# Performance work log

Measured on AMD Instinct MI355X. Metric: run time of the kernel, lower is better.

Reference implementation:

```python
import jax, jax.numpy as jnp
import numpy as np

SEF = 64   # skipped edge features (MLPGraphNetwork default sef)
SNF = 64   # skipped node features (MLPGraphNetwork default snf)
NR_STEPS = 3


def mlp2(x, W0, b0, W1, b1):
    # MyMLP with multI=1.0, relu hidden, linear last, no layernorm
    return jax.nn.relu(x @ W0 + b0) @ W1 + b1


def setup_inputs() -> dict:
    N, E = 50000, 800000
    nrNodeF, nrEdgeF, nrEmbed, nrTypes = 32, 3, 16, 2
    key = jax.random.key(0)
    ks = jax.random.split(key, 20)

    def w(k, fi, fo):
        # torch.normal(0,1) * (2.0 / fan_in)  (relu init in MyMLP)
        return jax.random.normal(k, (fi, fo), jnp.float32) * (2.0 / fi)

    z = lambda n: jnp.zeros((n,), jnp.float32)
    return {
        "edge_index": jax.random.randint(ks[0], (2, E), 0, N),
        "nodeFeatures": jax.random.uniform(ks[1], (N, nrNodeF), jnp.float32),
        "edgeFeatures": jax.random.normal(ks[2], (E, nrEdgeF), jnp.float32),
        "emb": jax.random.normal(ks[3], (nrTypes, nrEmbed), jnp.float32),
        "enc_n_W0": w(ks[4], nrNodeF - 1 + nrEmbed, 128), "enc_n_b0": z(128),
        "enc_n_W1": w(ks[5], 128, 128), "enc_n_b1": z(128),
        "enc_e_W0": w(ks[6], nrEdgeF, 128), "enc_e_b0": z(128),
        "enc_e_W1": w(ks[7], 128, 128), "enc_e_b1": z(128),
        "core_e_W0": w(ks[8], 192, 128), "core_e_b0": z(128),
        "core_e_W1": w(ks[9], 128, 64), "core_e_b1": z(64),
        "core_n_W0": w(ks[10], 128, 128), "core_n_b0": z(128),
        "core_n_W1": w(ks[11], 128, 64), "core_n_b1": z(64),
        "dec_W0": w(ks[12], 128, 128), "dec_b0": z(128),
        "dec_W1": w(ks[13], 128, 3), "dec_b1": z(3),
    }


def reference(edge_index, nodeFeatures, edgeFeatures, emb,
              enc_n_W0, enc_n_b0, enc_n_W1, enc_n_b1,
              enc_e_W0, enc_e_b0, enc_e_W1, enc_e_b1,
              core_e_W0, core_e_b0, core_e_W1, core_e_b1,
              core_n_W0, core_n_b0, core_n_W1, core_n_b1,
              dec_W0, dec_b0, dec_W1, dec_b1):
    N = nodeFeatures.shape[0]
    src, dst = edge_index[0], edge_index[1]  # j (source), i (target)

    # encode: embed particle type from last node feature column
    ptype = (nodeFeatures[:, -1] + 0.5).astype(jnp.int32)
    node = jnp.concatenate([nodeFeatures[:, :-1], emb[ptype]], axis=-1)
    node = mlp2(node, enc_n_W0, enc_n_b0, enc_n_W1, enc_n_b1)          # [N,128]
    edge = mlp2(edgeFeatures, enc_e_W0, enc_e_b0, enc_e_W1, enc_e_b1)  # [E,128]

    ones = jnp.ones((edge_index.shape[1],), node.dtype)
    counts = jnp.maximum(jax.ops.segment_sum(ones, dst, num_segments=N), 1.0)

    # process: shared MLPGraphNetwork applied NR_STEPS times
    for _ in range(NR_STEPS):
        einp = jnp.concatenate([edge[:, SEF:], node[dst][:, SNF:], node[src][:, SNF:]], axis=-1)  # [E,192]
        eout = mlp2(einp, core_e_W0, core_e_b0, core_e_W1, core_e_b1)  # [E,64]
        edge = jnp.concatenate([edge[:, :SEF], edge[:, SEF:] + eout], axis=-1)  # residual tail, [E,128]
        agg = jax.ops.segment_sum(edge, dst, num_segments=N) / counts[:, None]  # mean aggr, [N,128]
        ninp = jnp.concatenate([agg[:, SEF:], node[:, SNF:]], axis=-1)  # [N,128]
        nout = mlp2(ninp, core_n_W0, core_n_b0, core_n_W1, core_n_b1)  # [N,64]
        node = jnp.concatenate([node[:, :SNF], node[:, SNF:] + nout], axis=-1)  # [N,128]

    # decode
    return mlp2(node, dec_W0, dec_b0, dec_W1, dec_b1)  # [N,3]
```

## Files before the change

kernel.cpp:

```cpp
#include <hip/hip_runtime.h>
#include <cstdint>
#include <cstddef>


__global__ void k_zero(int* __restrict__ p, int n) {
    int i = blockIdx.x * 256 + threadIdx.x;
    if (i < n) p[i] = 0;
}


__global__ void k_hist(const int* __restrict__ dst, int* __restrict__ counts, int E) {
    int e = blockIdx.x * 256 + threadIdx.x;
    if (e < E) atomicAdd(&counts[dst[e]], 1);
}

__global__ __launch_bounds__(1024) void k_scan(
    const int* __restrict__ counts, int* __restrict__ row_off,
    int* __restrict__ cursor, float* __restrict__ inv_cnt, int N) {
    __shared__ int wsum[16];
    int t = threadIdx.x;
    int wave = t >> 6, lane = t & 63;
    int carry = 0;
    for (int base = 0; base < N; base += 1024) {
        int i = base + t;
        int v = (i < N) ? counts[i] : 0;
        int s = v;
        #pragma unroll
        for (int off = 1; off < 64; off <<= 1) {
            int u = __shfl_up(s, off, 64);
            if (lane >= off) s += u;
        }
        if (lane == 63) wsum[wave] = s;
        __syncthreads();
        int wpre = 0, full = 0;
        #pragma unroll
        for (int wv = 0; wv < 16; wv++) {
            int x = wsum[wv];
            full += x;
            if (wv < wave) wpre += x;
        }
        if (i < N) {
            int excl = carry + wpre + s - v;
            row_off[i] = excl;
            cursor[i]  = excl;
            inv_cnt[i] = 1.0f / (float)((v > 0) ? v : 1);
        }
        carry += full;
        __syncthreads();
    }
    if (t == 0) row_off[N] = carry;
}

__global__ void k_fill(const int* __restrict__ dst, int* __restrict__ cursor,
                       int* __restrict__ edge_list, int E) {
    int e = blockIdx.x * 256 + threadIdx.x;
    if (e < E) {
        int pos = atomicAdd(&cursor[dst[e]], 1);
        edge_list[pos] = e;
    }
}

__global__ void k_perm_idx(const int* __restrict__ elist,
                           const int* __restrict__ src, const int* __restrict__ dst,
                           int* __restrict__ src_p, int* __restrict__ dst_p, int E) {
    int i = blockIdx.x * 256 + threadIdx.x;
    if (i < E) {
        int e = elist[i];
        src_p[i] = src[e];
        dst_p[i] = dst[e];
    }
}


__global__ void k_embW(const float* __restrict__ emb, const float* __restrict__ W0,
                       const float* __restrict__ b0, float* __restrict__ embW) {
    int c = threadIdx.x;
    #pragma unroll
    for (int p = 0; p < 2; p++) {
        float acc = b0[c];
        #pragma unroll
        for (int k = 0; k < 16; k++)
            acc = fmaf(emb[p * 16 + k], W0[(31 + k) * 128 + c], acc);
        embW[p * 128 + c] = acc;
    }
}


__device__ __forceinline__ void g1_accum32(
    const float4* __restrict__ a4, int kk4,
    const float* __restrict__ W, int cbase, float* __restrict__ h) {
    #pragma clang loop unroll(disable)
    for (int kk = 0; kk < kk4; kk++) {
        float4 a = a4[kk];
        const float* wr = W + (size_t)kk * 4 * 128 + cbase;
        const float4* w0 = reinterpret_cast<const float4*>(wr);
        const float4* w1 = reinterpret_cast<const float4*>(wr + 128);
        const float4* w2 = reinterpret_cast<const float4*>(wr + 256);
        const float4* w3 = reinterpret_cast<const float4*>(wr + 384);
        #pragma unroll
        for (int cg = 0; cg < 8; cg++) {
            float4 p = w0[cg], q = w1[cg], r = w2[cg], s = w3[cg];
            h[cg*4+0] = fmaf(a.w, s.x, fmaf(a.z, r.x, fmaf(a.y, q.x, fmaf(a.x, p.x, h[cg*4+0]))));
            h[cg*4+1] = fmaf(a.w, s.y, fmaf(a.z, r.y, fmaf(a.y, q.y, fmaf(a.x, p.y, h[cg*4+1]))));
            h[cg*4+2] = fmaf(a.w, s.z, fmaf(a.z, r.z, fmaf(a.y, q.z, fmaf(a.x, p.z, h[cg*4+2]))));
            h[cg*4+3] = fmaf(a.w, s.w, fmaf(a.z, r.w, fmaf(a.y, q.w, fmaf(a.x, p.w, h[cg*4+3]))));
        }
    }
}

__device__ __forceinline__ void g1_tail3(
    float x, float y, float z, const float* __restrict__ W, int cbase,
    float* __restrict__ h) {
    const float4* w0 = reinterpret_cast<const float4*>(W + cbase);
    const float4* w1 = reinterpret_cast<const float4*>(W + 128 + cbase);
    const float4* w2 = reinterpret_cast<const float4*>(W + 256 + cbase);
    #pragma unroll
    for (int cg = 0; cg < 8; cg++) {
        float4 p = w0[cg], q = w1[cg], r = w2[cg];
        h[cg*4+0] = fmaf(z, r.x, fmaf(y, q.x, fmaf(x, p.x, h[cg*4+0])));
        h[cg*4+1] = fmaf(z, r.y, fmaf(y, q.y, fmaf(x, p.y, h[cg*4+1])));
        h[cg*4+2] = fmaf(z, r.z, fmaf(y, q.z, fmaf(x, p.z, h[cg*4+2])));
        h[cg*4+3] = fmaf(z, r.w, fmaf(y, q.w, fmaf(x, p.w, h[cg*4+3])));
    }
}

__device__ __forceinline__ void g2_accum64(
    float* __restrict__ sb, const float* __restrict__ hc,
    const float* __restrict__ W1, int kbase, int rs, float* __restrict__ o) {
    int t = threadIdx.x;
    #pragma unroll
    for (int k = 0; k < 32; k++) sb[k * 256 + t] = hc[k];
    __syncthreads();
    #pragma clang loop unroll(disable)
    for (int k = 0; k < 32; k++) {
        float hk = sb[k * 256 + t];
        const float4* w = reinterpret_cast<const float4*>(W1 + (size_t)(kbase + k) * rs);
        #pragma unroll
        for (int cg = 0; cg < 16; cg++) {
            float4 wv = w[cg];
            o[cg*4+0] = fmaf(hk, wv.x, o[cg*4+0]);
            o[cg*4+1] = fmaf(hk, wv.y, o[cg*4+1]);
            o[cg*4+2] = fmaf(hk, wv.z, o[cg*4+2]);
            o[cg*4+3] = fmaf(hk, wv.w, o[cg*4+3]);
        }
    }
    __syncthreads();
}


__global__ __launch_bounds__(256, 2) void k_enc_node_tail(
    const float* __restrict__ nodeF, const float* __restrict__ embW,
    const float* __restrict__ W0, const float* __restrict__ W1,
    const float* __restrict__ b1, float* __restrict__ nodeT, int N) {
    __shared__ float sb[32 * 256];
    int n = blockIdx.x * 256 + threadIdx.x;
    bool valid = n < N;
    int nc = valid ? n : N - 1;
    const float4* nf4 = reinterpret_cast<const float4*>(nodeF + (size_t)nc * 32);
    float4 v7 = nf4[7];
    int p = (int)(v7.w + 0.5f);
    const float4* ew = reinterpret_cast<const float4*>(embW + p * 128);

    float o[64];
    const float4* bv = reinterpret_cast<const float4*>(b1 + 64);
    #pragma unroll
    for (int i = 0; i < 16; i++) {
        float4 b = bv[i];
        o[4*i+0] = b.x; o[4*i+1] = b.y; o[4*i+2] = b.z; o[4*i+3] = b.w;
    }
    #pragma unroll
    for (int ch = 0; ch < 4; ch++) {
        int cbase = ch * 32;
        float h[32];
        #pragma unroll
        for (int i = 0; i < 8; i++) {
            float4 u = ew[ch*8 + i];
            h[4*i+0] = u.x; h[4*i+1] = u.y; h[4*i+2] = u.z; h[4*i+3] = u.w;
        }
        g1_accum32(nf4, 7, W0, cbase, h);
        g1_tail3(v7.x, v7.y, v7.z, W0 + 28*128, cbase, h);
        #pragma unroll
        for (int i = 0; i < 32; i++) h[i] = fmaxf(h[i], 0.0f);
        g2_accum64(sb, h, W1 + 64, cbase, 128, o);
    }
    if (valid) {
        float4* out4 = reinterpret_cast<float4*>(nodeT + (size_t)n * 64);
        #pragma unroll
        for (int i = 0; i < 16; i++)
            out4[i] = make_float4(o[4*i], o[4*i+1], o[4*i+2], o[4*i+3]);
    }
}


__global__ __launch_bounds__(256, 3) void k_enc_edge_T(
    const float* __restrict__ edgeF, const int* __restrict__ perm, int usePerm,
    const float* __restrict__ W0, const float* __restrict__ b0,
    const float* __restrict__ W1, const float* __restrict__ b1,
    float* __restrict__ edgeT, int E) {
    __shared__ float H[128 * 65];
    __shared__ float Wbuf[32 * 68];
    __shared__ float Xs[64 * 4];

    int t = threadIdx.x;
    int base = blockIdx.x * 64;

    if (t < 192) {
        int i = t / 3, j = t - i * 3;
        int e = base + i; int ec = (e < E) ? e : E - 1;
        int e2 = usePerm ? perm[ec] : ec;
        Xs[i * 4 + j] = edgeF[(size_t)e2 * 3 + j];
    }
    __syncthreads();

    int eg = t & 15, cg = t >> 4;
    float c1[4][8];
    {
        float4 b0a = *reinterpret_cast<const float4*>(b0 + cg * 8);
        float4 b0b = *reinterpret_cast<const float4*>(b0 + cg * 8 + 4);
        float bb[8] = {b0a.x,b0a.y,b0a.z,b0a.w,b0b.x,b0b.y,b0b.z,b0b.w};
        #pragma unroll
        for (int ie = 0; ie < 4; ie++)
            #pragma unroll
            for (int jc = 0; jc < 8; jc++) c1[ie][jc] = bb[jc];
    }
    #pragma unroll
    for (int k = 0; k < 3; k++) {
        float4 wa = *reinterpret_cast<const float4*>(W0 + k * 128 + cg * 8);
        float4 wb = *reinterpret_cast<const float4*>(W0 + k * 128 + cg * 8 + 4);
        float ww[8] = {wa.x,wa.y,wa.z,wa.w,wb.x,wb.y,wb.z,wb.w};
        #pragma unroll
        for (int ie = 0; ie < 4; ie++) {
            float a = Xs[(eg + 16 * ie) * 4 + k];
            #pragma unroll
            for (int jc = 0; jc < 8; jc++)
                c1[ie][jc] = fmaf(a, ww[jc], c1[ie][jc]);
        }
    }

    int wr_r = t >> 3, wr_cb = t & 7;
    float4 wreg2[2];
    {
        const float4* wr = reinterpret_cast<const float4*>(
            W1 + (size_t)(wr_r) * 128 + 64 + wr_cb * 8);
        wreg2[0] = wr[0]; wreg2[1] = wr[1];
    }

    #pragma unroll
    for (int ie = 0; ie < 4; ie++)
        #pragma unroll
        for (int jc = 0; jc < 8; jc++)
            H[(cg * 8 + jc) * 65 + eg + 16 * ie] = fmaxf(c1[ie][jc], 0.0f);

    int eg2 = t & 15, cg2 = t >> 4;
    float c2[4][4];
    {
        float4 bv = *reinterpret_cast<const float4*>(b1 + 64 + cg2 * 4);
        #pragma unroll
        for (int ie = 0; ie < 4; ie++) {
            c2[ie][0]=bv.x; c2[ie][1]=bv.y; c2[ie][2]=bv.z; c2[ie][3]=bv.w;
        }
    }
    #pragma clang loop unroll(disable)
    for (int phase = 0; phase < 4; phase++) {
        __syncthreads();
        {
            float* wd = Wbuf + wr_r * 68 + wr_cb * 8;
            wd[0]=wreg2[0].x; wd[1]=wreg2[0].y; wd[2]=wreg2[0].z; wd[3]=wreg2[0].w;
            wd[4]=wreg2[1].x; wd[5]=wreg2[1].y; wd[6]=wreg2[1].z; wd[7]=wreg2[1].w;
        }
        __syncthreads();
        if (phase < 3) {
            const float4* wr = reinterpret_cast<const float4*>(
                W1 + (size_t)((phase + 1) * 32 + wr_r) * 128 + 64 + wr_cb * 8);
            wreg2[0] = wr[0]; wreg2[1] = wr[1];
        }
        #pragma clang loop unroll_count(4)
        for (int k = 0; k < 32; k++) {
            int c = phase * 32 + k;
            float a0 = H[c*65 + eg2*4 + 0];
            float a1 = H[c*65 + eg2*4 + 1];
            float a2 = H[c*65 + eg2*4 + 2];
            float a3 = H[c*65 + eg2*4 + 3];
            float4 b4 = *reinterpret_cast<const float4*>(Wbuf + k * 68 + cg2 * 4);
            float bb[4] = {b4.x, b4.y, b4.z, b4.w};
            #pragma unroll
            for (int jc = 0; jc < 4; jc++) {
                c2[0][jc] = fmaf(a0, bb[jc], c2[0][jc]);
                c2[1][jc] = fmaf(a1, bb[jc], c2[1][jc]);
                c2[2][jc] = fmaf(a2, bb[jc], c2[2][jc]);
                c2[3][jc] = fmaf(a3, bb[jc], c2[3][jc]);
            }
        }
    }
    #pragma unroll
    for (int ie = 0; ie < 4; ie++) {
        int e = base + eg2 * 4 + ie;
        if (e < E) {
            *reinterpret_cast<float4*>(edgeT + (size_t)e * 64 + cg2 * 4) =
                make_float4(c2[ie][0], c2[ie][1], c2[ie][2], c2[ie][3]);
        }
    }
}


__global__ __launch_bounds__(256, 4) void k_node_pre_d(
    const float* __restrict__ nodeT, const float* __restrict__ W0,
    const float* __restrict__ b0, float* __restrict__ Pd, int N) {
    int n = blockIdx.x * 256 + threadIdx.x;
    bool valid = n < N;
    int nc = valid ? n : N - 1;
    const float4* a4 = reinterpret_cast<const float4*>(nodeT + (size_t)nc * 64);

    #pragma unroll
    for (int ch = 0; ch < 4; ch++) {
        int cbase = ch * 32;
        float h[32];
        const float4* b0v = reinterpret_cast<const float4*>(b0 + cbase);
        #pragma unroll
        for (int i = 0; i < 8; i++) {
            float4 b = b0v[i];
            h[4*i+0] = b.x; h[4*i+1] = b.y; h[4*i+2] = b.z; h[4*i+3] = b.w;
        }
        g1_accum32(a4, 16, W0 + 64*128, cbase, h);
        if (valid) {
            float4* o4 = reinterpret_cast<float4*>(Pd + (size_t)n * 128 + cbase);
            #pragma unroll
            for (int i = 0; i < 8; i++)
                o4[i] = make_float4(h[4*i], h[4*i+1], h[4*i+2], h[4*i+3]);
        }
    }
}


__global__ __launch_bounds__(256, 3) void k_edge_core_T(
    float* __restrict__ edgeT, const float* __restrict__ Pd,
    const float* __restrict__ nodeT,
    const int* __restrict__ srcI, const int* __restrict__ dstI,
    const float* __restrict__ W0, const float* __restrict__ W1,
    const float* __restrict__ b1, int E) {
    __shared__ float Abuf[2 * 64 * 65];
    __shared__ float Wbuf[32 * 132];

    int t = threadIdx.x;
    int base = blockIdx.x * 64;

    {
        int i = t >> 2, q = t & 3;
        int e = base + i; int ec = (e < E) ? e : E - 1;
        const float4* er = reinterpret_cast<const float4*>(edgeT + (size_t)ec * 64 + q * 16);
        int s = srcI[ec];
        const float4* sr = reinterpret_cast<const float4*>(nodeT + (size_t)s * 64 + q * 16);
        float* ae = Abuf + i * 65 + q * 16;
        float* as = Abuf + 64 * 65 + i * 65 + q * 16;
        #pragma unroll
        for (int j4 = 0; j4 < 4; j4++) {
            float4 v = er[j4];
            ae[j4*4+0]=v.x; ae[j4*4+1]=v.y; ae[j4*4+2]=v.z; ae[j4*4+3]=v.w;
            float4 w = sr[j4];
            as[j4*4+0]=w.x; as[j4*4+1]=w.y; as[j4*4+2]=w.z; as[j4*4+3]=w.w;
        }
    }

    int eg = t & 15, cg = t >> 4;
    float c1[4][8];
    #pragma unroll
    for (int ie = 0; ie < 4; ie++) {
        int e = base + eg + 16 * ie; int ec = (e < E) ? e : E - 1;
        int d = dstI[ec];
        const float4* pr = reinterpret_cast<const float4*>(Pd + (size_t)d * 128 + cg * 8);
        float4 p0 = pr[0], p1 = pr[1];
        c1[ie][0]=p0.x; c1[ie][1]=p0.y; c1[ie][2]=p0.z; c1[ie][3]=p0.w;
        c1[ie][4]=p1.x; c1[ie][5]=p1.y; c1[ie][6]=p1.z; c1[ie][7]=p1.w;
    }

    int wr_r = t >> 3, wr_cb = t & 7;
    float4 wreg[4];
    {
        const float4* wr = reinterpret_cast<const float4*>(
            W0 + (size_t)(0 + wr_r) * 128 + wr_cb * 16);
        wreg[0]=wr[0]; wreg[1]=wr[1]; wreg[2]=wr[2]; wreg[3]=wr[3];
    }
    #pragma clang loop unroll(disable)
    for (int phase = 0; phase < 4; phase++) {
        const float* Asrc = Abuf + ((phase < 2) ? 0 : 64 * 65);
        int koff = (phase & 1) * 32;
        __syncthreads();
        {
            float* wd = Wbuf + wr_r * 132 + wr_cb * 16;
            #pragma unroll
            for (int j4 = 0; j4 < 4; j4++) {
                wd[j4*4+0]=wreg[j4].x; wd[j4*4+1]=wreg[j4].y;
                wd[j4*4+2]=wreg[j4].z; wd[j4*4+3]=wreg[j4].w;
            }
        }
        __syncthreads();
        if (phase < 3) {
            int wrow_n = (phase + 1 < 2) ? (phase + 1) * 32 : 128 + (phase - 1) * 32;
            const float4* wr = reinterpret_cast<const float4*>(
                W0 + (size_t)(wrow_n + wr_r) * 128 + wr_cb * 16);
            wreg[0]=wr[0]; wreg[1]=wr[1]; wreg[2]=wr[2]; wreg[3]=wr[3];
        }
        #pragma clang loop unroll_count(4)
        for (int k = 0; k < 32; k++) {
            float a0 = Asrc[(eg + 16*0)*65 + koff + k];
            float a1 = Asrc[(eg + 16*1)*65 + koff + k];
            float a2 = Asrc[(eg + 16*2)*65 + koff + k];
            float a3 = Asrc[(eg + 16*3)*65 + koff + k];
            const float* wrp = Wbuf + k * 132 + cg * 8;
            float4 bq0 = *reinterpret_cast<const float4*>(wrp);
            float4 bq1 = *reinterpret_cast<const float4*>(wrp + 4);
            float bb[8] = {bq0.x,bq0.y,bq0.z,bq0.w,bq1.x,bq1.y,bq1.z,bq1.w};
            #pragma unroll
            for (int jc = 0; jc < 8; jc++) {
                c1[0][jc] = fmaf(a0, bb[jc], c1[0][jc]);
                c1[1][jc] = fmaf(a1, bb[jc], c1[1][jc]);
                c1[2][jc] = fmaf(a2, bb[jc], c1[2][jc]);
                c1[3][jc] = fmaf(a3, bb[jc], c1[3][jc]);
            }
        }
    }

    float4 wreg2[2];
    {
        const float4* wr = reinterpret_cast<const float4*>(
            W1 + (size_t)(wr_r) * 64 + wr_cb * 8);
        wreg2[0] = wr[0]; wreg2[1] = wr[1];
    }

    __syncthreads();
    float* H = Abuf;
    #pragma unroll
    for (int ie = 0; ie < 4; ie++)
        #pragma unroll
        for (int jc = 0; jc < 8; jc++)
            H[(cg*8 + jc) * 65 + eg + 16*ie] = fmaxf(c1[ie][jc], 0.0f);

    int eg2 = t & 15, cg2 = t >> 4;
    float c2[4][4];
    {
        float4 bv = *reinterpret_cast<const float4*>(b1 + cg2 * 4);
        #pragma unroll
        for (int ie = 0; ie < 4; ie++) {
            c2[ie][0]=bv.x; c2[ie][1]=bv.y; c2[ie][2]=bv.z; c2[ie][3]=bv.w;
        }
    }
    #pragma clang loop unroll(disable)
    for (int phase = 0; phase < 4; phase++) {
        __syncthreads();
        {
            float* wd = Wbuf + wr_r * 68 + wr_cb * 8;
            wd[0]=wreg2[0].x; wd[1]=wreg2[0].y; wd[2]=wreg2[0].z; wd[3]=wreg2[0].w;
            wd[4]=wreg2[1].x; wd[5]=wreg2[1].y; wd[6]=wreg2[1].z; wd[7]=wreg2[1].w;
        }
        __syncthreads();
        if (phase < 3) {
            const float4* wr = reinterpret_cast<const float4*>(
                W1 + (size_t)((phase + 1) * 32 + wr_r) * 64 + wr_cb * 8);
            wreg2[0] = wr[0]; wreg2[1] = wr[1];
        }
        #pragma clang loop unroll_count(4)
        for (int k = 0; k < 32; k++) {
            int c = phase * 32 + k;
            float a0 = H[c*65 + eg2*4 + 0];
            float a1 = H[c*65 + eg2*4 + 1];
            float a2 = H[c*65 + eg2*4 + 2];
            float a3 = H[c*65 + eg2*4 + 3];
            float4 b4 = *reinterpret_cast<const float4*>(Wbuf + k * 68 + cg2 * 4);
            float bb[4] = {b4.x, b4.y, b4.z, b4.w};
            #pragma unroll
            for (int jc = 0; jc < 4; jc++) {
                c2[0][jc] = fmaf(a0, bb[jc], c2[0][jc]);
                c2[1][jc] = fmaf(a1, bb[jc], c2[1][jc]);
                c2[2][jc] = fmaf(a2, bb[jc], c2[2][jc]);
                c2[3][jc] = fmaf(a3, bb[jc], c2[3][jc]);
            }
        }
    }

    #pragma unroll
    for (int ie = 0; ie < 4; ie++) {
        int e = base + eg2 * 4 + ie;
        if (e < E) {
            float4* er = reinterpret_cast<float4*>(edgeT + (size_t)e * 64 + cg2 * 4);
            float4 old = *er;
            old.x += c2[ie][0]; old.y += c2[ie][1];
            old.z += c2[ie][2]; old.w += c2[ie][3];
            *er = old;
        }
    }
}


__global__ __launch_bounds__(256, 3) void k_node_core_T(
    const float* __restrict__ aggT, float* __restrict__ nodeT,
    const float* __restrict__ W0, const float* __restrict__ b0,
    const float* __restrict__ W1, const float* __restrict__ b1, int N) {
    __shared__ float Abuf[64 * 132];
    __shared__ float Wbuf[32 * 132];

    int t = threadIdx.x;
    int base = blockIdx.x * 64;

    {
        int i = t >> 2, q = t & 3;
        int n = base + i; int nc = (n < N) ? n : N - 1;
        const float4* gr = reinterpret_cast<const float4*>(aggT + (size_t)nc * 64 + q * 16);
        const float4* tr = reinterpret_cast<const float4*>(nodeT + (size_t)nc * 64 + q * 16);
        float* ag = Abuf + i * 132 + q * 16;
        float* at = Abuf + i * 132 + 64 + q * 16;
        #pragma unroll
        for (int j4 = 0; j4 < 4; j4++) {
            float4 v = gr[j4];
            ag[j4*4+0]=v.x; ag[j4*4+1]=v.y; ag[j4*4+2]=v.z; ag[j4*4+3]=v.w;
            float4 w = tr[j4];
            at[j4*4+0]=w.x; at[j4*4+1]=w.y; at[j4*4+2]=w.z; at[j4*4+3]=w.w;
        }
    }

    int ng = t & 15, cg = t >> 4;
    float c1[4][8];
    {
        float4 b0a = *reinterpret_cast<const float4*>(b0 + cg * 8);
        float4 b0b = *reinterpret_cast<const float4*>(b0 + cg * 8 + 4);
        float bb[8] = {b0a.x,b0a.y,b0a.z,b0a.w,b0b.x,b0b.y,b0b.z,b0b.w};
        #pragma unroll
        for (int in = 0; in < 4; in++)
            #pragma unroll
            for (int jc = 0; jc < 8; jc++) c1[in][jc] = bb[jc];
    }

    int wr_r = t >> 3, wr_cb = t & 7;
    float4 wreg[4];
    {
        const float4* wr = reinterpret_cast<const float4*>(
            W0 + (size_t)(wr_r) * 128 + wr_cb * 16);
        wreg[0]=wr[0]; wreg[1]=wr[1]; wreg[2]=wr[2]; wreg[3]=wr[3];
    }
    #pragma clang loop unroll(disable)
    for (int phase = 0; phase < 4; phase++) {
        int koff = phase * 32;
        __syncthreads();
        {
            float* wd = Wbuf + wr_r * 132 + wr_cb * 16;
            #pragma unroll
            for (int j4 = 0; j4 < 4; j4++) {
                wd[j4*4+0]=wreg[j4].x; wd[j4*4+1]=wreg[j4].y;
                wd[j4*4+2]=wreg[j4].z; wd[j4*4+3]=wreg[j4].w;
            }
        }
        __syncthreads();
        if (phase < 3) {
            const float4* wr = reinterpret_cast<const float4*>(
                W0 + (size_t)((phase + 1) * 32 + wr_r) * 128 + wr_cb * 16);
            wreg[0]=wr[0]; wreg[1]=wr[1]; wreg[2]=wr[2]; wreg[3]=wr[3];
        }
        #pragma clang loop unroll_count(4)
        for (int k = 0; k < 32; k++) {
            float a0 = Abuf[(ng + 16*0)*132 + koff + k];
            float a1 = Abuf[(ng + 16*1)*132 + koff + k];
            float a2 = Abuf[(ng + 16*2)*132 + koff + k];
            float a3 = Abuf[(ng + 16*3)*132 + koff + k];
            const float* wrp = Wbuf + k * 132 + cg * 8;
            float4 bq0 = *reinterpret_cast<const float4*>(wrp);
            float4 bq1 = *reinterpret_cast<const float4*>(wrp + 4);
            float bb[8] = {bq0.x,bq0.y,bq0.z,bq0.w,bq1.x,bq1.y,bq1.z,bq1.w};
            #pragma unroll
            for (int jc = 0; jc < 8; jc++) {
                c1[0][jc] = fmaf(a0, bb[jc], c1[0][jc]);
                c1[1][jc] = fmaf(a1, bb[jc], c1[1][jc]);
                c1[2][jc] = fmaf(a2, bb[jc], c1[2][jc]);
                c1[3][jc] = fmaf(a3, bb[jc], c1[3][jc]);
            }
        }
    }

    float4 wreg2[2];
    {
        const float4* wr = reinterpret_cast<const float4*>(
            W1 + (size_t)(wr_r) * 64 + wr_cb * 8);
        wreg2[0] = wr[0]; wreg2[1] = wr[1];
    }

    __syncthreads();
    float* H = Abuf;
    #pragma unroll
    for (int in = 0; in < 4; in++)
        #pragma unroll
        for (int jc = 0; jc < 8; jc++)
            H[(cg*8 + jc) * 65 + ng + 16*in] = fmaxf(c1[in][jc], 0.0f);

    int ng2 = t & 15, cg2 = t >> 4;
    float c2[4][4];
    {
        float4 bv = *reinterpret_cast<const float4*>(b1 + cg2 * 4);
        #pragma unroll
        for (int in = 0; in < 4; in++) {
            c2[in][0]=bv.x; c2[in][1]=bv.y; c2[in][2]=bv.z; c2[in][3]=bv.w;
        }
    }
    #pragma clang loop unroll(disable)
    for (int phase = 0; phase < 4; phase++) {
        __syncthreads();
        {
            float* wd = Wbuf + wr_r * 68 + wr_cb * 8;
            wd[0]=wreg2[0].x; wd[1]=wreg2[0].y; wd[2]=wreg2[0].z; wd[3]=wreg2[0].w;
            wd[4]=wreg2[1].x; wd[5]=wreg2[1].y; wd[6]=wreg2[1].z; wd[7]=wreg2[1].w;
        }
        __syncthreads();
        if (phase < 3) {
            const float4* wr = reinterpret_cast<const float4*>(
                W1 + (size_t)((phase + 1) * 32 + wr_r) * 64 + wr_cb * 8);
            wreg2[0] = wr[0]; wreg2[1] = wr[1];
        }
        #pragma clang loop unroll_count(4)
        for (int k = 0; k < 32; k++) {
            int c = phase * 32 + k;
            float a0 = H[c*65 + ng2*4 + 0];
            float a1 = H[c*65 + ng2*4 + 1];
            float a2 = H[c*65 + ng2*4 + 2];
            float a3 = H[c*65 + ng2*4 + 3];
            float4 b4 = *reinterpret_cast<const float4*>(Wbuf + k * 68 + cg2 * 4);
            float bb[4] = {b4.x, b4.y, b4.z, b4.w};
            #pragma unroll
            for (int jc = 0; jc < 4; jc++) {
                c2[0][jc] = fmaf(a0, bb[jc], c2[0][jc]);
                c2[1][jc] = fmaf(a1, bb[jc], c2[1][jc]);
                c2[2][jc] = fmaf(a2, bb[jc], c2[2][jc]);
                c2[3][jc] = fmaf(a3, bb[jc], c2[3][jc]);
            }
        }
    }

    #pragma unroll
    for (int in = 0; in < 4; in++) {
        int n = base + ng2 * 4 + in;
        if (n < N) {
            float4* nr = reinterpret_cast<float4*>(nodeT + (size_t)n * 64 + cg2 * 4);
            float4 old = *nr;
            old.x += c2[in][0]; old.y += c2[in][1];
            old.z += c2[in][2]; old.w += c2[in][3];
            *nr = old;
        }
    }
}


__global__ __launch_bounds__(256, 2) void k_edge_core_B(
    float* __restrict__ edgeT, const float* __restrict__ nodeT,
    const int* __restrict__ src, const int* __restrict__ dst,
    const float* __restrict__ W0, const float* __restrict__ b0,
    const float* __restrict__ W1, const float* __restrict__ b1, int E) {
    __shared__ float sb[32 * 256];
    int e = blockIdx.x * 256 + threadIdx.x;
    bool valid = e < E;
    int ec = valid ? e : E - 1;
    int d = dst[ec], s = src[ec];
    const float4* a4 = reinterpret_cast<const float4*>(edgeT + (size_t)ec * 64);
    const float4* d4 = reinterpret_cast<const float4*>(nodeT + (size_t)d * 64);
    const float4* s4 = reinterpret_cast<const float4*>(nodeT + (size_t)s * 64);

    float o[64];
    const float4* bv = reinterpret_cast<const float4*>(b1);
    #pragma unroll
    for (int i = 0; i < 16; i++) {
        float4 b = bv[i];
        o[4*i+0] = b.x; o[4*i+1] = b.y; o[4*i+2] = b.z; o[4*i+3] = b.w;
    }
    #pragma unroll
    for (int ch = 0; ch < 4; ch++) {
        int cbase = ch * 32;
        float h[32];
        const float4* b0v = reinterpret_cast<const float4*>(b0 + cbase);
        #pragma unroll
        for (int i = 0; i < 8; i++) {
            float4 b = b0v[i];
            h[4*i+0] = b.x; h[4*i+1] = b.y; h[4*i+2] = b.z; h[4*i+3] = b.w;
        }
        g1_accum32(a4, 16, W0, cbase, h);
        g1_accum32(d4, 16, W0 + 64*128, cbase, h);
        g1_accum32(s4, 16, W0 + 128*128, cbase, h);
        #pragma unroll
        for (int i = 0; i < 32; i++) h[i] = fmaxf(h[i], 0.0f);
        g2_accum64(sb, h, W1, cbase, 64, o);
    }
    if (valid) {
        float4* eo4 = reinterpret_cast<float4*>(edgeT + (size_t)e * 64);
        #pragma unroll
        for (int i = 0; i < 16; i++) {
            float4 t = a4[i];
            t.x += o[4*i+0]; t.y += o[4*i+1];
            t.z += o[4*i+2]; t.w += o[4*i+3];
            eo4[i] = t;
        }
    }
}


__global__ __launch_bounds__(256) void k_agg_csr(
    const float* __restrict__ edgeT, const int* __restrict__ row_off,
    const float* __restrict__ inv_cnt, float* __restrict__ aggT, int N) {
    int n = blockIdx.x * 4 + (threadIdx.x >> 6);
    int lane = threadIdx.x & 63;
    if (n >= N) return;
    int beg = row_off[n], end = row_off[n + 1];
    double s = 0.0;
    for (int idx = beg; idx < end; idx++)
        s += (double)edgeT[(size_t)idx * 64 + lane];
    aggT[(size_t)n * 64 + lane] = (float)(s * (double)inv_cnt[n]);
}

__global__ __launch_bounds__(256) void k_agg_gather(
    const float* __restrict__ edgeT, const int* __restrict__ row_off,
    const int* __restrict__ edge_list, const float* __restrict__ inv_cnt,
    float* __restrict__ aggT, int N) {
    int n = blockIdx.x * 4 + (threadIdx.x >> 6);
    int lane = threadIdx.x & 63;
    if (n >= N) return;
    int beg = row_off[n], end = row_off[n + 1];
    double s = 0.0;
    for (int idx = beg; idx < end; idx++) {
        int e = edge_list[idx];
        s += (double)edgeT[(size_t)e * 64 + lane];
    }
    aggT[(size_t)n * 64 + lane] = (float)(s * (double)inv_cnt[n]);
}


__global__ __launch_bounds__(256, 2) void k_decode(
    const float* __restrict__ nodeF, const float* __restrict__ embW,
    const float* __restrict__ encW0, const float* __restrict__ encW1,
    const float* __restrict__ encb1, const float* __restrict__ nodeT,
    const float* __restrict__ W0, const float* __restrict__ b0,
    const float* __restrict__ W1, const float* __restrict__ b1,
    float* __restrict__ out, int N) {
    __shared__ float sb[64 * 256];
    int t = threadIdx.x;
    int n = blockIdx.x * 256 + t;
    bool valid = n < N;
    int nc = valid ? n : N - 1;
    const float4* nf4 = reinterpret_cast<const float4*>(nodeF + (size_t)nc * 32);
    const float4* t4  = reinterpret_cast<const float4*>(nodeT + (size_t)nc * 64);
    float4 v7 = nf4[7];
    int p = (int)(v7.w + 0.5f);
    const float4* ew = reinterpret_cast<const float4*>(embW + p * 128);

    float head[64];
    const float4* ebv = reinterpret_cast<const float4*>(encb1);
    #pragma unroll
    for (int i = 0; i < 16; i++) {
        float4 b = ebv[i];
        head[4*i+0] = b.x; head[4*i+1] = b.y; head[4*i+2] = b.z; head[4*i+3] = b.w;
    }
    #pragma unroll
    for (int ch = 0; ch < 4; ch++) {
        int cbase = ch * 32;
        float h[32];
        #pragma unroll
        for (int i = 0; i < 8; i++) {
            float4 u = ew[ch*8 + i];
            h[4*i+0] = u.x; h[4*i+1] = u.y; h[4*i+2] = u.z; h[4*i+3] = u.w;
        }
        g1_accum32(nf4, 7, encW0, cbase, h);
        g1_tail3(v7.x, v7.y, v7.z, encW0 + 28*128, cbase, h);
        #pragma unroll
        for (int i = 0; i < 32; i++) h[i] = fmaxf(h[i], 0.0f);
        g2_accum64(sb, h, encW1, cbase, 128, head);
    }

    #pragma unroll
    for (int k = 0; k < 64; k++) sb[k * 256 + t] = head[k];
    __syncthreads();

    float h2[128];
    #pragma unroll
    for (int ch = 0; ch < 4; ch++) {
        int cbase = ch * 32;
        float* hc = &h2[ch * 32];
        const float4* b0v = reinterpret_cast<const float4*>(b0 + cbase);
        #pragma unroll
        for (int i = 0; i < 8; i++) {
            float4 b = b0v[i];
            hc[4*i+0] = b.x; hc[4*i+1] = b.y; hc[4*i+2] = b.z; hc[4*i+3] = b.w;
        }
        #pragma clang loop unroll(disable)
        for (int k = 0; k < 64; k++) {
            float hk = sb[k * 256 + t];
            const float4* w = reinterpret_cast<const float4*>(W0 + (size_t)k * 128 + cbase);
            #pragma unroll
            for (int cg = 0; cg < 8; cg++) {
                float4 wv = w[cg];
                hc[cg*4+0] = fmaf(hk, wv.x, hc[cg*4+0]);
                hc[cg*4+1] = fmaf(hk, wv.y, hc[cg*4+1]);
                hc[cg*4+2] = fmaf(hk, wv.z, hc[cg*4+2]);
                hc[cg*4+3] = fmaf(hk, wv.w, hc[cg*4+3]);
            }
        }
        g1_accum32(t4, 16, W0 + 64*128, cbase, hc);
    }
    __syncthreads();

    float o0 = b1[0], o1 = b1[1], o2 = b1[2];
    #pragma unroll
    for (int ch = 0; ch < 4; ch++) {
        int kb = ch * 32;
        #pragma unroll
        for (int k = 0; k < 32; k++) sb[k * 256 + t] = fmaxf(h2[kb + k], 0.0f);
        __syncthreads();
        #pragma clang loop unroll(disable)
        for (int k = 0; k < 32; k++) {
            float hk = sb[k * 256 + t];
            const float* w = W1 + (size_t)(kb + k) * 3;
            o0 = fmaf(hk, w[0], o0);
            o1 = fmaf(hk, w[1], o1);
            o2 = fmaf(hk, w[2], o2);
        }
        __syncthreads();
    }
    if (valid) {
        out[(size_t)n * 3 + 0] = o0;
        out[(size_t)n * 3 + 1] = o1;
        out[(size_t)n * 3 + 2] = o2;
    }
}


extern "C" void kernel_launch(void* const* d_in, const int* in_sizes, int n_in,
                              void* d_out, int out_size, void* d_ws, size_t ws_size,
                              hipStream_t stream) {
    const int*   edge_index = (const int*)  d_in[0];
    const float* nodeF      = (const float*)d_in[1];
    const float* edgeF      = (const float*)d_in[2];
    const float* emb        = (const float*)d_in[3];
    const float* enc_n_W0   = (const float*)d_in[4];
    const float* enc_n_b0   = (const float*)d_in[5];
    const float* enc_n_W1   = (const float*)d_in[6];
    const float* enc_n_b1   = (const float*)d_in[7];
    const float* enc_e_W0   = (const float*)d_in[8];
    const float* enc_e_b0   = (const float*)d_in[9];
    const float* enc_e_W1   = (const float*)d_in[10];
    const float* enc_e_b1   = (const float*)d_in[11];
    const float* core_e_W0  = (const float*)d_in[12];
    const float* core_e_b0  = (const float*)d_in[13];
    const float* core_e_W1  = (const float*)d_in[14];
    const float* core_e_b1  = (const float*)d_in[15];
    const float* core_n_W0  = (const float*)d_in[16];
    const float* core_n_b0  = (const float*)d_in[17];
    const float* core_n_W1  = (const float*)d_in[18];
    const float* core_n_b1  = (const float*)d_in[19];
    const float* dec_W0     = (const float*)d_in[20];
    const float* dec_b0     = (const float*)d_in[21];
    const float* dec_W1     = (const float*)d_in[22];
    const float* dec_b1     = (const float*)d_in[23];
    (void)n_in; (void)out_size;

    const int E = in_sizes[0] / 2;
    const int N = in_sizes[1] / 32;
    const int* src = edge_index;
    const int* dst = edge_index + E;

    auto al = [](size_t x) { return (x + 255) & ~(size_t)255; };
    const size_t szEdgeT = al((size_t)E * 64 * 4);
    const size_t szNodeT = al((size_t)N * 64 * 4);
    const size_t szP     = al((size_t)N * 128 * 4);
    const size_t szAgg   = al((size_t)N * 64 * 4);
    const size_t szElist = al((size_t)E * 4);
    const size_t szN4    = al((size_t)N * 4);
    const size_t szRow   = al((size_t)(N + 1) * 4);
    const size_t szEmbW  = al(2 * 128 * 4);
    const size_t base = szEdgeT + szNodeT + szElist + szRow + 3 * szN4 + szEmbW;
    const size_t needCSR = base + 2 * szElist + szP;
    const size_t needAp  = base + szP;
    const int plan = (ws_size >= needCSR) ? 0 : (ws_size >= needAp) ? 1 : 2;

    char* ws = (char*)d_ws;
    size_t off = 0;
    auto carve = [&](size_t bytes) -> char* { char* p = ws + off; off += bytes; return p; };
    float* edgeT   = (float*)carve(szEdgeT);
    float* nodeT   = (float*)carve(szNodeT);
    int*   elist   = (int*)  carve(szElist);
    int*   row_off = (int*)  carve(szRow);
    int*   counts  = (int*)  carve(szN4);
    int*   cursor  = (int*)  carve(szN4);
    float* inv_cnt = (float*)carve(szN4);
    float* embW    = (float*)carve(szEmbW);
    int *src_p = nullptr, *dst_p = nullptr;
    float *Pd = nullptr, *aggT = nullptr;
    if (plan == 0) {
        src_p = (int*)carve(szElist);
        dst_p = (int*)carve(szElist);
        Pd = (float*)carve(szP); aggT = Pd;
    } else if (plan == 1) {
        Pd = (float*)carve(szP); aggT = Pd;
    } else {
        aggT = (float*)carve(szAgg);
    }

    int blkE = (E + 255) / 256;
    int blkN = (N + 255) / 256;
    int blkT = (E + 63) / 64;
    int blkNT = (N + 63) / 64;

    k_zero<<<(N + 255) / 256, 256, 0, stream>>>(counts, N);
    k_hist<<<blkE, 256, 0, stream>>>(dst, counts, E);
    k_scan<<<1, 1024, 0, stream>>>(counts, row_off, cursor, inv_cnt, N);
    k_fill<<<blkE, 256, 0, stream>>>(dst, cursor, elist, E);
    if (plan == 0)
        k_perm_idx<<<blkE, 256, 0, stream>>>(elist, src, dst, src_p, dst_p, E);

    k_embW<<<1, 128, 0, stream>>>(emb, enc_n_W0, enc_n_b0, embW);
    k_enc_node_tail<<<blkN, 256, 0, stream>>>(nodeF, embW, enc_n_W0, enc_n_W1,
                                              enc_n_b1, nodeT, N);
    k_enc_edge_T<<<blkT, 256, 0, stream>>>(edgeF, elist, (plan == 0) ? 1 : 0,
                                           enc_e_W0, enc_e_b0, enc_e_W1, enc_e_b1,
                                           edgeT, E);

    for (int step = 0; step < 3; step++) {
        if (plan == 0) {
            k_node_pre_d<<<blkN, 256, 0, stream>>>(nodeT, core_e_W0, core_e_b0, Pd, N);
            k_edge_core_T<<<blkT, 256, 0, stream>>>(edgeT, Pd, nodeT, src_p, dst_p,
                                                    core_e_W0, core_e_W1, core_e_b1, E);
            k_agg_csr<<<(N + 3) / 4, 256, 0, stream>>>(edgeT, row_off, inv_cnt, aggT, N);
        } else if (plan == 1) {
            k_node_pre_d<<<blkN, 256, 0, stream>>>(nodeT, core_e_W0, core_e_b0, Pd, N);
            k_edge_core_T<<<blkT, 256, 0, stream>>>(edgeT, Pd, nodeT, src, dst,
                                                    core_e_W0, core_e_W1, core_e_b1, E);
            k_agg_gather<<<(N + 3) / 4, 256, 0, stream>>>(edgeT, row_off, elist,
                                                          inv_cnt, aggT, N);
        } else {
            k_edge_core_B<<<blkE, 256, 0, stream>>>(edgeT, nodeT, src, dst,
                                                    core_e_W0, core_e_b0,
                                                    core_e_W1, core_e_b1, E);
            k_agg_gather<<<(N + 3) / 4, 256, 0, stream>>>(edgeT, row_off, elist,
                                                          inv_cnt, aggT, N);
        }
        k_node_core_T<<<blkNT, 256, 0, stream>>>(aggT, nodeT, core_n_W0, core_n_b0,
                                                 core_n_W1, core_n_b1, N);
    }
    k_decode<<<blkN, 256, 0, stream>>>(nodeF, embW, enc_n_W0, enc_n_W1, enc_n_b1,
                                       nodeT, dec_W0, dec_b0, dec_W1, dec_b1,
                                       (float*)d_out, N);
}
```

Measured before the change: 2.859 ms.

## Pad shared tiles to 68/136 strides for float4 LDS reads; halve second-GEMM phases

Shared-memory row strides change from 65/132 to 68 (and 136 for the node Abuf allocation), so activation and hidden tiles can be read and written as aligned float4 vectors instead of scalar loads. The first GEMM in the edge and node core kernels now loads four k-values per row as one float4, and the second GEMM uses 64-row weight staging in two phases instead of four, which halves its barriers. The intent is to cut LDS instruction count and synchronization in the inner loops. The larger shared buffers raise LDS per block and may reduce occupancy. The node kernel allocates Abuf with stride 136 but still indexes it with 132; that is still in bounds and 16-byte aligned.

```diff
diff --git a/kernel.cpp b/kernel.cpp
--- a/kernel.cpp
+++ b/kernel.cpp
@@ -2,6 +2,10 @@
 #include <cstdint>
 #include <cstddef>
 
+
+__device__ __forceinline__ float f4c(const float4& v, int k) {
+    return k == 0 ? v.x : (k == 1 ? v.y : (k == 2 ? v.z : v.w));
+}
 
 __global__ void k_zero(int* __restrict__ p, int n) {
     int i = blockIdx.x * 256 + threadIdx.x;
@@ -197,8 +201,8 @@
     const float* __restrict__ W0, const float* __restrict__ b0,
     const float* __restrict__ W1, const float* __restrict__ b1,
     float* __restrict__ edgeT, int E) {
-    __shared__ float H[128 * 65];
-    __shared__ float Wbuf[32 * 68];
+    __shared__ float H[128 * 68];
+    __shared__ float Wbuf[64 * 68];
     __shared__ float Xs[64 * 4];
 
     int t = threadIdx.x;
@@ -237,19 +241,19 @@
         }
     }
 
-    int wr_r = t >> 3, wr_cb = t & 7;
-    float4 wreg2[2];
+    int r2 = t >> 2, cb2 = t & 3;
+    float4 wreg2[4];
     {
         const float4* wr = reinterpret_cast<const float4*>(
-            W1 + (size_t)(wr_r) * 128 + 64 + wr_cb * 8);
-        wreg2[0] = wr[0]; wreg2[1] = wr[1];
+            W1 + (size_t)r2 * 128 + 64 + cb2 * 16);
+        wreg2[0]=wr[0]; wreg2[1]=wr[1]; wreg2[2]=wr[2]; wreg2[3]=wr[3];
     }
 
     #pragma unroll
     for (int ie = 0; ie < 4; ie++)
         #pragma unroll
         for (int jc = 0; jc < 8; jc++)
-            H[(cg * 8 + jc) * 65 + eg + 16 * ie] = fmaxf(c1[ie][jc], 0.0f);
+            H[(cg * 8 + jc) * 68 + eg + 16 * ie] = fmaxf(c1[ie][jc], 0.0f);
 
     int eg2 = t & 15, cg2 = t >> 4;
     float c2[4][4];
@@ -261,34 +265,31 @@
         }
     }
     #pragma clang loop unroll(disable)
-    for (int phase = 0; phase < 4; phase++) {
+    for (int phase = 0; phase < 2; phase++) {
         __syncthreads();
         {
-            float* wd = Wbuf + wr_r * 68 + wr_cb * 8;
-            wd[0]=wreg2[0].x; wd[1]=wreg2[0].y; wd[2]=wreg2[0].z; wd[3]=wreg2[0].w;
-            wd[4]=wreg2[1].x; wd[5]=wreg2[1].y; wd[6]=wreg2[1].z; wd[7]=wreg2[1].w;
-        }
-        __syncthreads();
-        if (phase < 3) {
+            float4* wd = reinterpret_cast<float4*>(Wbuf + r2 * 68 + cb2 * 16);
+            wd[0]=wreg2[0]; wd[1]=wreg2[1]; wd[2]=wreg2[2]; wd[3]=wreg2[3];
+        }
+        __syncthreads();
+        if (phase < 1) {
             const float4* wr = reinterpret_cast<const float4*>(
-                W1 + (size_t)((phase + 1) * 32 + wr_r) * 128 + 64 + wr_cb * 8);
-            wreg2[0] = wr[0]; wreg2[1] = wr[1];
+                W1 + (size_t)(64 + r2) * 128 + 64 + cb2 * 16);
+            wreg2[0]=wr[0]; wreg2[1]=wr[1]; wreg2[2]=wr[2]; wreg2[3]=wr[3];
         }
         #pragma clang loop unroll_count(4)
-        for (int k = 0; k < 32; k++) {
-            int c = phase * 32 + k;
-            float a0 = H[c*65 + eg2*4 + 0];
-            float a1 = H[c*65 + eg2*4 + 1];
-            float a2 = H[c*65 + eg2*4 + 2];
-            float a3 = H[c*65 + eg2*4 + 3];
+        for (int k = 0; k < 64; k++) {
+            int c = phase * 64 + k;
+            float4 av = *reinterpret_cast<const float4*>(H + c * 68 + eg2 * 4);
             float4 b4 = *reinterpret_cast<const float4*>(Wbuf + k * 68 + cg2 * 4);
             float bb[4] = {b4.x, b4.y, b4.z, b4.w};
+            float aa[4] = {av.x, av.y, av.z, av.w};
             #pragma unroll
             for (int jc = 0; jc < 4; jc++) {
-                c2[0][jc] = fmaf(a0, bb[jc], c2[0][jc]);
-                c2[1][jc] = fmaf(a1, bb[jc], c2[1][jc]);
-                c2[2][jc] = fmaf(a2, bb[jc], c2[2][jc]);
-                c2[3][jc] = fmaf(a3, bb[jc], c2[3][jc]);
+                c2[0][jc] = fmaf(aa[0], bb[jc], c2[0][jc]);
+                c2[1][jc] = fmaf(aa[1], bb[jc], c2[1][jc]);
+                c2[2][jc] = fmaf(aa[2], bb[jc], c2[2][jc]);
+                c2[3][jc] = fmaf(aa[3], bb[jc], c2[3][jc]);
             }
         }
     }
@@ -338,8 +339,8 @@
     const int* __restrict__ srcI, const int* __restrict__ dstI,
     const float* __restrict__ W0, const float* __restrict__ W1,
     const float* __restrict__ b1, int E) {
-    __shared__ float Abuf[2 * 64 * 65];
-    __shared__ float Wbuf[32 * 132];
+    __shared__ float Abuf[2 * 64 * 68];
+    __shared__ float Wbuf[64 * 68];
 
     int t = threadIdx.x;
     int base = blockIdx.x * 64;
@@ -350,15 +351,10 @@
         const float4* er = reinterpret_cast<const float4*>(edgeT + (size_t)ec * 64 + q * 16);
         int s = srcI[ec];
         const float4* sr = reinterpret_cast<const float4*>(nodeT + (size_t)s * 64 + q * 16);
-        float* ae = Abuf + i * 65 + q * 16;
-        float* as = Abuf + 64 * 65 + i * 65 + q * 16;
-        #pragma unroll
-        for (int j4 = 0; j4 < 4; j4++) {
-            float4 v = er[j4];
-            ae[j4*4+0]=v.x; ae[j4*4+1]=v.y; ae[j4*4+2]=v.z; ae[j4*4+3]=v.w;
-            float4 w = sr[j4];
-            as[j4*4+0]=w.x; as[j4*4+1]=w.y; as[j4*4+2]=w.z; as[j4*4+3]=w.w;
-        }
+        float4* ae = reinterpret_cast<float4*>(Abuf + i * 68 + q * 16);
+        float4* as = reinterpret_cast<float4*>(Abuf + 64 * 68 + i * 68 + q * 16);
+        #pragma unroll
+        for (int j4 = 0; j4 < 4; j4++) { ae[j4] = er[j4]; as[j4] = sr[j4]; }
     }
 
     int eg = t & 15, cg = t >> 4;
@@ -377,21 +373,17 @@
     float4 wreg[4];
     {
         const float4* wr = reinterpret_cast<const float4*>(
-            W0 + (size_t)(0 + wr_r) * 128 + wr_cb * 16);
+            W0 + (size_t)wr_r * 128 + wr_cb * 16);
         wreg[0]=wr[0]; wreg[1]=wr[1]; wreg[2]=wr[2]; wreg[3]=wr[3];
     }
     #pragma clang loop unroll(disable)
     for (int phase = 0; phase < 4; phase++) {
-        const float* Asrc = Abuf + ((phase < 2) ? 0 : 64 * 65);
+        const float* Asrc = Abuf + ((phase < 2) ? 0 : 64 * 68);
         int koff = (phase & 1) * 32;
         __syncthreads();
         {
-            float* wd = Wbuf + wr_r * 132 + wr_cb * 16;
-            #pragma unroll
-            for (int j4 = 0; j4 < 4; j4++) {
-                wd[j4*4+0]=wreg[j4].x; wd[j4*4+1]=wreg[j4].y;
-                wd[j4*4+2]=wreg[j4].z; wd[j4*4+3]=wreg[j4].w;
-            }
+            float4* wd = reinterpret_cast<float4*>(Wbuf + wr_r * 132 + wr_cb * 16);
+            wd[0]=wreg[0]; wd[1]=wreg[1]; wd[2]=wreg[2]; wd[3]=wreg[3];
         }
         __syncthreads();
         if (phase < 3) {
@@ -400,31 +392,38 @@
                 W0 + (size_t)(wrow_n + wr_r) * 128 + wr_cb * 16);
             wreg[0]=wr[0]; wreg[1]=wr[1]; wreg[2]=wr[2]; wreg[3]=wr[3];
         }
-        #pragma clang loop unroll_count(4)
-        for (int k = 0; k < 32; k++) {
-            float a0 = Asrc[(eg + 16*0)*65 + koff + k];
-            float a1 = Asrc[(eg + 16*1)*65 + koff + k];
-            float a2 = Asrc[(eg + 16*2)*65 + koff + k];
-            float a3 = Asrc[(eg + 16*3)*65 + koff + k];
-            const float* wrp = Wbuf + k * 132 + cg * 8;
-            float4 bq0 = *reinterpret_cast<const float4*>(wrp);
-            float4 bq1 = *reinterpret_cast<const float4*>(wrp + 4);
-            float bb[8] = {bq0.x,bq0.y,bq0.z,bq0.w,bq1.x,bq1.y,bq1.z,bq1.w};
-            #pragma unroll
-            for (int jc = 0; jc < 8; jc++) {
-                c1[0][jc] = fmaf(a0, bb[jc], c1[0][jc]);
-                c1[1][jc] = fmaf(a1, bb[jc], c1[1][jc]);
-                c1[2][jc] = fmaf(a2, bb[jc], c1[2][jc]);
-                c1[3][jc] = fmaf(a3, bb[jc], c1[3][jc]);
+        #pragma clang loop unroll_count(2)
+        for (int k4 = 0; k4 < 8; k4++) {
+            float4 av[4];
+            #pragma unroll
+            for (int ie = 0; ie < 4; ie++)
+                av[ie] = *reinterpret_cast<const float4*>(
+                    Asrc + (eg + 16 * ie) * 68 + koff + k4 * 4);
+            #pragma unroll
+            for (int kk = 0; kk < 4; kk++) {
+                const float* wrp = Wbuf + (k4 * 4 + kk) * 132 + cg * 8;
+                float4 bq0 = *reinterpret_cast<const float4*>(wrp);
+                float4 bq1 = *reinterpret_cast<const float4*>(wrp + 4);
+                float bb[8] = {bq0.x,bq0.y,bq0.z,bq0.w,bq1.x,bq1.y,bq1.z,bq1.w};
+                float a0 = f4c(av[0], kk), a1 = f4c(av[1], kk);
+                float a2 = f4c(av[2], kk), a3 = f4c(av[3], kk);
+                #pragma unroll
+                for (int jc = 0; jc < 8; jc++) {
+                    c1[0][jc] = fmaf(a0, bb[jc], c1[0][jc]);
+                    c1[1][jc] = fmaf(a1, bb[jc], c1[1][jc]);
+                    c1[2][jc] = fmaf(a2, bb[jc], c1[2][jc]);
+                    c1[3][jc] = fmaf(a3, bb[jc], c1[3][jc]);
+                }
             }
         }
     }
 
-    float4 wreg2[2];
+    int r2 = t >> 2, cb2 = t & 3;
+    float4 wreg2[4];
     {
         const float4* wr = reinterpret_cast<const float4*>(
-            W1 + (size_t)(wr_r) * 64 + wr_cb * 8);
-        wreg2[0] = wr[0]; wreg2[1] = wr[1];
+            W1 + (size_t)r2 * 64 + cb2 * 16);
+        wreg2[0]=wr[0]; wreg2[1]=wr[1]; wreg2[2]=wr[2]; wreg2[3]=wr[3];
     }
 
     __syncthreads();
@@ -433,7 +432,7 @@
     for (int ie = 0; ie < 4; ie++)
         #pragma unroll
         for (int jc = 0; jc < 8; jc++)
-            H[(cg*8 + jc) * 65 + eg + 16*ie] = fmaxf(c1[ie][jc], 0.0f);
+            H[(cg*8 + jc) * 68 + eg + 16*ie] = fmaxf(c1[ie][jc], 0.0f);
 
     int eg2 = t & 15, cg2 = t >> 4;
     float c2[4][4];
@@ -445,34 +444,31 @@
         }
     }
     #pragma clang loop unroll(disable)
-    for (int phase = 0; phase < 4; phase++) {
+    for (int phase = 0; phase < 2; phase++) {
         __syncthreads();
         {
-            float* wd = Wbuf + wr_r * 68 + wr_cb * 8;
-            wd[0]=wreg2[0].x; wd[1]=wreg2[0].y; wd[2]=wreg2[0].z; wd[3]=wreg2[0].w;
-            wd[4]=wreg2[1].x; wd[5]=wreg2[1].y; wd[6]=wreg2[1].z; wd[7]=wreg2[1].w;
-        }
-        __syncthreads();
-        if (phase < 3) {
+            float4* wd = reinterpret_cast<float4*>(Wbuf + r2 * 68 + cb2 * 16);
+            wd[0]=wreg2[0]; wd[1]=wreg2[1]; wd[2]=wreg2[2]; wd[3]=wreg2[3];
+        }
+        __syncthreads();
+        if (phase < 1) {
             const float4* wr = reinterpret_cast<const float4*>(
-                W1 + (size_t)((phase + 1) * 32 + wr_r) * 64 + wr_cb * 8);
-            wreg2[0] = wr[0]; wreg2[1] = wr[1];
+                W1 + (size_t)(64 + r2) * 64 + cb2 * 16);
+            wreg2[0]=wr[0]; wreg2[1]=wr[1]; wreg2[2]=wr[2]; wreg2[3]=wr[3];
         }
         #pragma clang loop unroll_count(4)
-        for (int k = 0; k < 32; k++) {
-            int c = phase * 32 + k;
-            float a0 = H[c*65 + eg2*4 + 0];
-            float a1 = H[c*65 + eg2*4 + 1];
-            float a2 = H[c*65 + eg2*4 + 2];
-            float a3 = H[c*65 + eg2*4 + 3];
+        for (int k = 0; k < 64; k++) {
+            int c = phase * 64 + k;
+            float4 av = *reinterpret_cast<const float4*>(H + c * 68 + eg2 * 4);
             float4 b4 = *reinterpret_cast<const float4*>(Wbuf + k * 68 + cg2 * 4);
             float bb[4] = {b4.x, b4.y, b4.z, b4.w};
+            float aa[4] = {av.x, av.y, av.z, av.w};
             #pragma unroll
             for (int jc = 0; jc < 4; jc++) {
-                c2[0][jc] = fmaf(a0, bb[jc], c2[0][jc]);
-                c2[1][jc] = fmaf(a1, bb[jc], c2[1][jc]);
-                c2[2][jc] = fmaf(a2, bb[jc], c2[2][jc]);
-                c2[3][jc] = fmaf(a3, bb[jc], c2[3][jc]);
+                c2[0][jc] = fmaf(aa[0], bb[jc], c2[0][jc]);
+                c2[1][jc] = fmaf(aa[1], bb[jc], c2[1][jc]);
+                c2[2][jc] = fmaf(aa[2], bb[jc], c2[2][jc]);
+                c2[3][jc] = fmaf(aa[3], bb[jc], c2[3][jc]);
             }
         }
     }
@@ -495,8 +491,8 @@
     const float* __restrict__ aggT, float* __restrict__ nodeT,
     const float* __restrict__ W0, const float* __restrict__ b0,
     const float* __restrict__ W1, const float* __restrict__ b1, int N) {
-    __shared__ float Abuf[64 * 132];
-    __shared__ float Wbuf[32 * 132];
+    __shared__ float Abuf[64 * 136];
+    __shared__ float Wbuf[64 * 68];
 
     int t = threadIdx.x;
     int base = blockIdx.x * 64;
@@ -506,15 +502,10 @@
         int n = base + i; int nc = (n < N) ? n : N - 1;
         const float4* gr = reinterpret_cast<const float4*>(aggT + (size_t)nc * 64 + q * 16);
         const float4* tr = reinterpret_cast<const float4*>(nodeT + (size_t)nc * 64 + q * 16);
-        float* ag = Abuf + i * 132 + q * 16;
-        float* at = Abuf + i * 132 + 64 + q * 16;
-        #pragma unroll
-        for (int j4 = 0; j4 < 4; j4++) {
-            float4 v = gr[j4];
-            ag[j4*4+0]=v.x; ag[j4*4+1]=v.y; ag[j4*4+2]=v.z; ag[j4*4+3]=v.w;
-            float4 w = tr[j4];
-            at[j4*4+0]=w.x; at[j4*4+1]=w.y; at[j4*4+2]=w.z; at[j4*4+3]=w.w;
-        }
+        float4* ag = reinterpret_cast<float4*>(Abuf + i * 132 + q * 16);
+        float4* at = reinterpret_cast<float4*>(Abuf + i * 132 + 64 + q * 16);
+        #pragma unroll
+        for (int j4 = 0; j4 < 4; j4++) { ag[j4] = gr[j4]; at[j4] = tr[j4]; }
     }
 
     int ng = t & 15, cg = t >> 4;
@@ -533,7 +524,7 @@
     float4 wreg[4];
     {
         const float4* wr = reinterpret_cast<const float4*>(
-            W0 + (size_t)(wr_r) * 128 + wr_cb * 16);
+            W0 + (size_t)wr_r * 128 + wr_cb * 16);
         wreg[0]=wr[0]; wreg[1]=wr[1]; wreg[2]=wr[2]; wreg[3]=wr[3];
     }
     #pragma clang loop unroll(disable)
@@ -541,12 +532,8 @@
         int koff = phase * 32;
         __syncthreads();
         {
-            float* wd = Wbuf + wr_r * 132 + wr_cb * 16;
-            #pragma unroll
-            for (int j4 = 0; j4 < 4; j4++) {
-                wd[j4*4+0]=wreg[j4].x; wd[j4*4+1]=wreg[j4].y;
-                wd[j4*4+2]=wreg[j4].z; wd[j4*4+3]=wreg[j4].w;
-            }
+            float4* wd = reinterpret_cast<float4*>(Wbuf + wr_r * 132 + wr_cb * 16);
+            wd[0]=wreg[0]; wd[1]=wreg[1]; wd[2]=wreg[2]; wd[3]=wreg[3];
         }
         __syncthreads();
         if (phase < 3) {
@@ -554,31 +541,38 @@
                 W0 + (size_t)((phase + 1) * 32 + wr_r) * 128 + wr_cb * 16);
             wreg[0]=wr[0]; wreg[1]=wr[1]; wreg[2]=wr[2]; wreg[3]=wr[3];
         }
-        #pragma clang loop unroll_count(4)
-        for (int k = 0; k < 32; k++) {
-            float a0 = Abuf[(ng + 16*0)*132 + koff + k];
-            float a1 = Abuf[(ng + 16*1)*132 + koff + k];
-            float a2 = Abuf[(ng + 16*2)*132 + koff + k];
-            float a3 = Abuf[(ng + 16*3)*132 + koff + k];
-            const float* wrp = Wbuf + k * 132 + cg * 8;
-            float4 bq0 = *reinterpret_cast<const float4*>(wrp);
-            float4 bq1 = *reinterpret_cast<const float4*>(wrp + 4);
-            float bb[8] = {bq0.x,bq0.y,bq0.z,bq0.w,bq1.x,bq1.y,bq1.z,bq1.w};
-            #pragma unroll
-            for (int jc = 0; jc < 8; jc++) {
-                c1[0][jc] = fmaf(a0, bb[jc], c1[0][jc]);
-                c1[1][jc] = fmaf(a1, bb[jc], c1[1][jc]);
-                c1[2][jc] = fmaf(a2, bb[jc], c1[2][jc]);
-                c1[3][jc] = fmaf(a3, bb[jc], c1[3][jc]);
+        #pragma clang loop unroll_count(2)
+        for (int k4 = 0; k4 < 8; k4++) {
+            float4 av[4];
+            #pragma unroll
+            for (int in = 0; in < 4; in++)
+                av[in] = *reinterpret_cast<const float4*>(
+                    Abuf + (ng + 16 * in) * 132 + koff + k4 * 4);
+            #pragma unroll
+            for (int kk = 0; kk < 4; kk++) {
+                const float* wrp = Wbuf + (k4 * 4 + kk) * 132 + cg * 8;
+                float4 bq0 = *reinterpret_cast<const float4*>(wrp);
+                float4 bq1 = *reinterpret_cast<const float4*>(wrp + 4);
+                float bb[8] = {bq0.x,bq0.y,bq0.z,bq0.w,bq1.x,bq1.y,bq1.z,bq1.w};
+                float a0 = f4c(av[0], kk), a1 = f4c(av[1], kk);
+                float a2 = f4c(av[2], kk), a3 = f4c(av[3], kk);
+                #pragma unroll
+                for (int jc = 0; jc < 8; jc++) {
+                    c1[0][jc] = fmaf(a0, bb[jc], c1[0][jc]);
+                    c1[1][jc] = fmaf(a1, bb[jc], c1[1][jc]);
+                    c1[2][jc] = fmaf(a2, bb[jc], c1[2][jc]);
+                    c1[3][jc] = fmaf(a3, bb[jc], c1[3][jc]);
+                }
             }
         }
     }
 
-    float4 wreg2[2];
+    int r2 = t >> 2, cb2 = t & 3;
+    float4 wreg2[4];
     {
         const float4* wr = reinterpret_cast<const float4*>(
-            W1 + (size_t)(wr_r) * 64 + wr_cb * 8);
-        wreg2[0] = wr[0]; wreg2[1] = wr[1];
+            W1 + (size_t)r2 * 64 + cb2 * 16);
+        wreg2[0]=wr[0]; wreg2[1]=wr[1]; wreg2[2]=wr[2]; wreg2[3]=wr[3];
     }
 
     __syncthreads();
@@ -587,7 +581,7 @@
     for (int in = 0; in < 4; in++)
         #pragma unroll
         for (int jc = 0; jc < 8; jc++)
-            H[(cg*8 + jc) * 65 + ng + 16*in] = fmaxf(c1[in][jc], 0.0f);
+            H[(cg*8 + jc) * 68 + ng + 16*in] = fmaxf(c1[in][jc], 0.0f);
 
     int ng2 = t & 15, cg2 = t >> 4;
     float c2[4][4];
@@ -599,34 +593,31 @@
         }
     }
     #pragma clang loop unroll(disable)
-    for (int phase = 0; phase < 4; phase++) {
+    for (int phase = 0; phase < 2; phase++) {
         __syncthreads();
         {
-            float* wd = Wbuf + wr_r * 68 + wr_cb * 8;
-            wd[0]=wreg2[0].x; wd[1]=wreg2[0].y; wd[2]=wreg2[0].z; wd[3]=wreg2[0].w;
-            wd[4]=wreg2[1].x; wd[5]=wreg2[1].y; wd[6]=wreg2[1].z; wd[7]=wreg2[1].w;
-        }
-        __syncthreads();
-        if (phase < 3) {
+            float4* wd = reinterpret_cast<float4*>(Wbuf + r2 * 68 + cb2 * 16);
+            wd[0]=wreg2[0]; wd[1]=wreg2[1]; wd[2]=wreg2[2]; wd[3]=wreg2[3];
+        }
+        __syncthreads();
+        if (phase < 1) {
             const float4* wr = reinterpret_cast<const float4*>(
-                W1 + (size_t)((phase + 1) * 32 + wr_r) * 64 + wr_cb * 8);
-            wreg2[0] = wr[0]; wreg2[1] = wr[1];
+                W1 + (size_t)(64 + r2) * 64 + cb2 * 16);
+            wreg2[0]=wr[0]; wreg2[1]=wr[1]; wreg2[2]=wr[2]; wreg2[3]=wr[3];
         }
         #pragma clang loop unroll_count(4)
-        for (int k = 0; k < 32; k++) {
-            int c = phase * 32 + k;
-            float a0 = H[c*65 + ng2*4 + 0];
-            float a1 = H[c*65 + ng2*4 + 1];
-            float a2 = H[c*65 + ng2*4 + 2];
-            float a3 = H[c*65 + ng2*4 + 3];
+        for (int k = 0; k < 64; k++) {
+            int c = phase * 64 + k;
+            float4 av = *reinterpret_cast<const float4*>(H + c * 68 + ng2 * 4);
             float4 b4 = *reinterpret_cast<const float4*>(Wbuf + k * 68 + cg2 * 4);
             float bb[4] = {b4.x, b4.y, b4.z, b4.w};
+            float aa[4] = {av.x, av.y, av.z, av.w};
             #pragma unroll
             for (int jc = 0; jc < 4; jc++) {
-                c2[0][jc] = fmaf(a0, bb[jc], c2[0][jc]);
-                c2[1][jc] = fmaf(a1, bb[jc], c2[1][jc]);
-                c2[2][jc] = fmaf(a2, bb[jc], c2[2][jc]);
-                c2[3][jc] = fmaf(a3, bb[jc], c2[3][jc]);
+                c2[0][jc] = fmaf(aa[0], bb[jc], c2[0][jc]);
+                c2[1][jc] = fmaf(aa[1], bb[jc], c2[1][jc]);
+                c2[2][jc] = fmaf(aa[2], bb[jc], c2[2][jc]);
+                c2[3][jc] = fmaf(aa[3], bb[jc], c2[3][jc]);
             }
         }
     }
```

Result: slower. 3.078 ms (+7.7%).
